# Optimization experiments

Hardware: AMD Instinct MI355X
Metric: run time of the kernel (lower is better)

Reference implementation:

```python
import jax, jax.numpy as jnp
import numpy as np

EPS = 1e-12  # matches torch F.normalize default eps (clamp_min)
B, C, N = 32, 512, 4096
K_CLUSTERS, G_CLUSTERS = 64, 8
T_CLUSTERS = K_CLUSTERS + G_CLUSTERS  # 72
H_ATTN = T_CLUSTERS // 4  # 18


def _l2norm(v, axis):
    return v / jnp.maximum(jnp.linalg.norm(v, axis=axis, keepdims=True), EPS)


def setup_inputs() -> dict:
    key = jax.random.key(0)
    ks = jax.random.split(key, 6)
    x = jax.random.normal(ks[0], (B, C, N), dtype=jnp.float32)
    centroids = jax.random.normal(ks[1], (T_CLUSTERS, C), dtype=jnp.float32) * 0.01
    # 1x1 Conv2d(C -> T) == dense [T, C] weight + bias
    conv_w = jax.random.normal(ks[2], (T_CLUSTERS, C), dtype=jnp.float32) / np.sqrt(C).astype(np.float32)
    conv_b = jnp.zeros((T_CLUSTERS,), dtype=jnp.float32)
    ghost_weights = jnp.ones((G_CLUSTERS,), dtype=jnp.float32) * 0.1
    w1 = jax.random.normal(ks[3], (H_ATTN, T_CLUSTERS), dtype=jnp.float32) / np.sqrt(T_CLUSTERS).astype(np.float32)
    b1 = jnp.zeros((H_ATTN,), dtype=jnp.float32)
    w2 = jax.random.normal(ks[4], (T_CLUSTERS, H_ATTN), dtype=jnp.float32) / np.sqrt(H_ATTN).astype(np.float32)
    b2 = jnp.zeros((T_CLUSTERS,), dtype=jnp.float32)
    return {"x": x, "centroids": centroids, "conv_w": conv_w, "conv_b": conv_b,
            "ghost_weights": ghost_weights, "w1": w1, "b1": b1, "w2": w2, "b2": b2}


def reference(x, centroids, conv_w, conv_b, ghost_weights, w1, b1, w2, b2):
    # x: [B, C, N] -> L2 normalize over channel dim
    xn = _l2norm(x, axis=1)
    # 1x1 conv -> soft assignment logits [B, T, N], softmax over clusters
    logits = jnp.einsum('kc,bcn->bkn', conv_w, xn) + conv_b[None, :, None]
    assign = jax.nn.softmax(logits, axis=1)
    # residual aggregation, algebraically fused:
    # vlad[b,k,c] = sum_n a[b,k,n]*x[b,c,n] - centroid[k,c]*sum_n a[b,k,n]
    agg = jnp.einsum('bkn,bcn->bkc', assign, xn)
    mass = assign.sum(axis=-1)  # [B, T]
    vlad = agg - centroids[None, :, :] * mass[:, :, None]
    # ghost cluster down-weighting
    gw = jax.nn.softmax(ghost_weights)
    vlad = vlad.at[:, K_CLUSTERS:, :].multiply(gw[None, :, None])
    # attention over clusters: mean over C -> MLP -> softmax over clusters
    scores = vlad.mean(axis=-1)  # [B, T]
    h = jax.nn.relu(scores @ w1.T + b1)
    attn = jax.nn.softmax(h @ w2.T + b2, axis=1)
    vlad = vlad * attn[:, :, None]
    # intra-cluster L2 norm, drop ghosts, flatten, global L2 norm
    vlad = _l2norm(vlad, axis=2)
    vlad = vlad[:, :K_CLUSTERS, :].reshape(vlad.shape[0], -1)
    return _l2norm(vlad, axis=1)
```

## Files before the change

### kernel.cpp

```cpp
#include <hip/hip_runtime.h>
#include <hip/hip_bf16.h>

#define B_ 32
#define C_ 512
#define N_ 4096
#define T_ 72
#define K_ 64
#define KP 80
#define EPSF 1e-12f

typedef unsigned short u16;
typedef unsigned int u32;
typedef __attribute__((ext_vector_type(8))) short bf16x8;
typedef __attribute__((ext_vector_type(4))) float f32x4;

__device__ __forceinline__ u16 f2bf(float v) {
    __hip_bfloat16 h = __float2bfloat16(v);
    return *reinterpret_cast<u16*>(&h);
}

__global__ __launch_bounds__(256) void k_prep(
    const float* __restrict__ conv_w, const float* __restrict__ conv_b,
    u16* __restrict__ Wp, float* __restrict__ bp)
{
    const int idx = blockIdx.x * 256 + threadIdx.x;
    if (idx < KP * C_) {
        const int k = idx >> 9, c = idx & (C_ - 1);
        Wp[idx] = f2bf(k < T_ ? conv_w[k * C_ + c] : 0.f);
    } else if (idx < KP * C_ + KP) {
        const int j = idx - KP * C_;
        bp[j] = (j < T_) ? conv_b[j] : -1e30f;
    }
}

#define ANW 256
__global__ __launch_bounds__(256, 2) void k_assign(
    const float* __restrict__ x, const u16* __restrict__ Wp,
    const float* __restrict__ bp, u16* __restrict__ assignp,
    float* __restrict__ mass)
{
    __shared__ u16   xs[ANW * 32];
    __shared__ float red[4][ANW];
    __shared__ float inv_sh[ANW];

    const int t = threadIdx.x;
    const int b = blockIdx.y;
    const int n0 = blockIdx.x * ANW;
    const int lane = t & 63, w = t >> 6;
    const int q = lane >> 4, nl = lane & 15;

    const float* xb = x + (size_t)b * C_ * N_ + n0 + 4 * lane;

    f32x4 acc[4][5];
    #pragma unroll
    for (int nt = 0; nt < 4; ++nt)
        #pragma unroll
        for (int mt = 0; mt < 5; ++mt) acc[nt][mt] = (f32x4)0.f;
    float ss[4] = {0.f, 0.f, 0.f, 0.f};

    float4 v[8];
    bf16x8 af[5];
    #pragma unroll
    for (int i = 0; i < 8; ++i)
        v[i] = *(const float4*)(xb + (size_t)(w * 8 + i) * N_);
    #pragma unroll
    for (int mt = 0; mt < 5; ++mt)
        af[mt] = *(const bf16x8*)(Wp + (size_t)(mt * 16 + nl) * C_ + q * 8);

#define VJ(i) (j == 0 ? v[i].x : j == 1 ? v[i].y : j == 2 ? v[i].z : v[i].w)

    #pragma unroll 1
    for (int ch = 0; ch < 16; ++ch) {
        #pragma unroll
        for (int j = 0; j < 4; ++j) {
            const float f0 = VJ(0), f1 = VJ(1), f2 = VJ(2), f3 = VJ(3);
            const float f4 = VJ(4), f5 = VJ(5), f6 = VJ(6), f7 = VJ(7);
            ss[j] = fmaf(f0, f0, ss[j]); ss[j] = fmaf(f1, f1, ss[j]);
            ss[j] = fmaf(f2, f2, ss[j]); ss[j] = fmaf(f3, f3, ss[j]);
            ss[j] = fmaf(f4, f4, ss[j]); ss[j] = fmaf(f5, f5, ss[j]);
            ss[j] = fmaf(f6, f6, ss[j]); ss[j] = fmaf(f7, f7, ss[j]);
            uint4 pk;
            pk.x = (u32)f2bf(f0) | ((u32)f2bf(f1) << 16);
            pk.y = (u32)f2bf(f2) | ((u32)f2bf(f3) << 16);
            pk.z = (u32)f2bf(f4) | ((u32)f2bf(f5) << 16);
            pk.w = (u32)f2bf(f6) | ((u32)f2bf(f7) << 16);
            const int n = 4 * lane + j;
            const int slot = (w + ((lane >> 1) & 3)) & 3;
            *(uint4*)&xs[n * 32 + slot * 8] = pk;
        }
        __syncthreads();
        if (ch < 15) {
            #pragma unroll
            for (int i = 0; i < 8; ++i)
                v[i] = *(const float4*)(xb + (size_t)((ch + 1) * 32 + w * 8 + i) * N_);
        }
        __builtin_amdgcn_sched_barrier(0);
        #pragma unroll
        for (int nt = 0; nt < 4; ++nt) {
            const int n = (4 * w + nt) * 16 + nl;
            const int slot = (q + ((n >> 3) & 3)) & 3;
            const bf16x8 bfr = *(const bf16x8*)&xs[n * 32 + slot * 8];
            #pragma unroll
            for (int mt = 0; mt < 5; ++mt)
                acc[nt][mt] = __builtin_amdgcn_mfma_f32_16x16x32_bf16(af[mt], bfr, acc[nt][mt], 0, 0, 0);
        }
        if (ch < 15) {
            #pragma unroll
            for (int mt = 0; mt < 5; ++mt)
                af[mt] = *(const bf16x8*)(Wp + (size_t)(mt * 16 + nl) * C_ + (ch + 1) * 32 + q * 8);
        }
        __syncthreads();
    }
#undef VJ

    *(float4*)&red[w][4 * lane] = make_float4(ss[0], ss[1], ss[2], ss[3]);
    __syncthreads();
    {
        const float s = red[0][t] + red[1][t] + red[2][t] + red[3][t];
        inv_sh[t] = 1.0f / fmaxf(sqrtf(s), EPSF);
    }
    __syncthreads();

    float bpv[5][4];
    #pragma unroll
    for (int mt = 0; mt < 5; ++mt)
        #pragma unroll
        for (int r = 0; r < 4; ++r) bpv[mt][r] = bp[mt * 16 + q * 4 + r];

    #pragma unroll
    for (int nt = 0; nt < 4; ++nt) {
        const int n_loc = (4 * w + nt) * 16 + nl;
        const float invn = inv_sh[n_loc];
        const int nglob = n0 + n_loc;

        float lg[5][4];
        #pragma unroll
        for (int mt = 0; mt < 5; ++mt)
            #pragma unroll
            for (int r = 0; r < 4; ++r)
                lg[mt][r] = acc[nt][mt][r] * invn + bpv[mt][r];

        float mx = -1e30f;
        #pragma unroll
        for (int mt = 0; mt < 5; ++mt)
            #pragma unroll
            for (int r = 0; r < 4; ++r) mx = fmaxf(mx, lg[mt][r]);
        mx = fmaxf(mx, __shfl_xor(mx, 16, 64));
        mx = fmaxf(mx, __shfl_xor(mx, 32, 64));

        float s = 0.f;
        #pragma unroll
        for (int mt = 0; mt < 5; ++mt)
            #pragma unroll
            for (int r = 0; r < 4; ++r) {
                lg[mt][r] = __expf(lg[mt][r] - mx);
                s += lg[mt][r];
            }
        s += __shfl_xor(s, 16, 64);
        s += __shfl_xor(s, 32, 64);
        const float rs = 1.0f / s;

        #pragma unroll
        for (int mt = 0; mt < 4; ++mt)
            #pragma unroll
            for (int r = 0; r < 4; ++r) {
                const float a = lg[mt][r] * rs;
                float msum = a;
                msum += __shfl_xor(msum, 1, 64);
                msum += __shfl_xor(msum, 2, 64);
                msum += __shfl_xor(msum, 4, 64);
                msum += __shfl_xor(msum, 8, 64);
                const int k = mt * 16 + q * 4 + r;
                if (nl == 0) atomicAdd(&mass[b * K_ + k], msum);
                assignp[((size_t)b * K_ + k) * N_ + nglob] = f2bf(a * invn);
            }
    }
}

#define AGW 1024
#define AGS 128
#define AGP 136
__global__ __launch_bounds__(256) void k_agg(
    const float* __restrict__ x, const u16* __restrict__ assignp,
    float* __restrict__ out)
{
    __shared__ u16 At[K_][AGP];
    __shared__ u16 Bt[K_][AGP];

    const int t = threadIdx.x, b = blockIdx.z;
    const int nc0 = blockIdx.y * AGW;
    const int c0 = blockIdx.x * 64;
    const int lane = t & 63, w = t >> 6;
    const int q = lane >> 4, nl = lane & 15;

    const int as = lane & 15, ar = lane >> 4;
    const int bs = lane & 31, br = lane >> 5;

    f32x4 acc[4];
    #pragma unroll
    for (int mt = 0; mt < 4; ++mt) acc[mt] = (f32x4)0.f;

    const u16*   ab = assignp + (size_t)b * K_ * N_;
    const float* xb = x + ((size_t)b * C_ + c0) * N_;

    uint4  ra[4];
    float4 rb[8];
    #pragma unroll
    for (int i = 0; i < 4; ++i)
        ra[i] = *(const uint4*)(ab + (size_t)(16 * w + 4 * i + ar) * N_ + nc0 + as * 8);
    #pragma unroll
    for (int i = 0; i < 8; ++i)
        rb[i] = *(const float4*)(xb + (size_t)(16 * w + 2 * i + br) * N_ + nc0 + bs * 4);

    #pragma unroll 1
    for (int ph = 0; ph < AGW / AGS; ++ph) {
        #pragma unroll
        for (int i = 0; i < 4; ++i)
            *(uint4*)&At[16 * w + 4 * i + ar][as * 8] = ra[i];
        #pragma unroll
        for (int i = 0; i < 8; ++i) {
            const float4 vv = rb[i];
            uint2 pk;
            pk.x = (u32)f2bf(vv.x) | ((u32)f2bf(vv.y) << 16);
            pk.y = (u32)f2bf(vv.z) | ((u32)f2bf(vv.w) << 16);
            *(uint2*)&Bt[16 * w + 2 * i + br][bs * 4] = pk;
        }
        __syncthreads();
        if (ph < AGW / AGS - 1) {
            const int n1 = nc0 + (ph + 1) * AGS;
            #pragma unroll
            for (int i = 0; i < 4; ++i)
                ra[i] = *(const uint4*)(ab + (size_t)(16 * w + 4 * i + ar) * N_ + n1 + as * 8);
            #pragma unroll
            for (int i = 0; i < 8; ++i)
                rb[i] = *(const float4*)(xb + (size_t)(16 * w + 2 * i + br) * N_ + n1 + bs * 4);
        }
        __builtin_amdgcn_sched_barrier(0);
        #pragma unroll
        for (int ks = 0; ks < 4; ++ks) {
            const bf16x8 bfr = *(const bf16x8*)&Bt[16 * w + nl][ks * 32 + q * 8];
            #pragma unroll
            for (int mt = 0; mt < 4; ++mt) {
                const bf16x8 afv = *(const bf16x8*)&At[mt * 16 + nl][ks * 32 + q * 8];
                acc[mt] = __builtin_amdgcn_mfma_f32_16x16x32_bf16(afv, bfr, acc[mt], 0, 0, 0);
            }
        }
        __syncthreads();
    }

    float* ob = out + (size_t)b * K_ * C_;
    const int c = c0 + 16 * w + nl;
    #pragma unroll
    for (int mt = 0; mt < 4; ++mt)
        #pragma unroll
        for (int r = 0; r < 4; ++r)
            atomicAdd(&ob[(size_t)(mt * 16 + q * 4 + r) * C_ + c], acc[mt][r]);
}

__device__ __forceinline__ float block_reduce_sum_256(float v) {
    #pragma unroll
    for (int o = 32; o > 0; o >>= 1) v += __shfl_down(v, o, 64);
    __shared__ float wsh[4];
    const int lane = threadIdx.x & 63, wid = threadIdx.x >> 6;
    if (lane == 0) wsh[wid] = v;
    __syncthreads();
    float r = 0.f;
    if (threadIdx.x == 0) r = wsh[0] + wsh[1] + wsh[2] + wsh[3];
    return r;
}

__global__ __launch_bounds__(256) void k_rnorm(
    const float* __restrict__ agg, const float* __restrict__ centroids,
    const float* __restrict__ mass, float* __restrict__ rnorm,
    float* __restrict__ gsum)
{
    const int k = blockIdx.x, b = blockIdx.y;
    const float mk = mass[b * K_ + k];
    const float* p  = agg + ((size_t)b * K_ + k) * C_;
    const float* cb = centroids + k * C_;
    float s = 0.f;
    #pragma unroll 2
    for (int i = threadIdx.x; i < C_; i += 256) {
        const float v = fmaf(-cb[i], mk, p[i]);
        s = fmaf(v, v, s);
    }
    const float ss = block_reduce_sum_256(s);
    if (threadIdx.x == 0) {
        const float rn = fmaxf(sqrtf(ss), EPSF);
        rnorm[b * K_ + k] = rn;
        atomicAdd(gsum + b, ss / (rn * rn));
    }
}

__global__ __launch_bounds__(256) void k_final(
    float* __restrict__ out, const float* __restrict__ centroids,
    const float* __restrict__ mass, const float* __restrict__ rnorm,
    const float* __restrict__ gsum)
{
    const size_t i4 = ((size_t)blockIdx.x * 256 + threadIdx.x) * 4;
    const int b = (int)(i4 >> 15);
    const int k = (int)((i4 >> 9) & 63);
    const int c = (int)(i4 & 511);
    const float gn = fmaxf(sqrtf(gsum[b]), EPSF);
    const float sc = 1.0f / (rnorm[b * K_ + k] * gn);
    const float mk = mass[b * K_ + k];
    float4 v  = *(const float4*)(out + i4);
    const float4 cv = *(const float4*)(centroids + k * C_ + c);
    v.x = fmaf(-cv.x, mk, v.x) * sc;
    v.y = fmaf(-cv.y, mk, v.y) * sc;
    v.z = fmaf(-cv.z, mk, v.z) * sc;
    v.w = fmaf(-cv.w, mk, v.w) * sc;
    *(float4*)(out + i4) = v;
}

extern "C" void kernel_launch(void* const* d_in, const int* in_sizes, int n_in,
                              void* d_out, int out_size, void* d_ws, size_t ws_size,
                              hipStream_t stream) {
    const float* x         = (const float*)d_in[0];
    const float* centroids = (const float*)d_in[1];
    const float* conv_w    = (const float*)d_in[2];
    const float* conv_b    = (const float*)d_in[3];

    float* out = (float*)d_out;
    char*  ws  = (char*)d_ws;

    u16*   assignp = (u16*)ws;
    u16*   Wp      = (u16*)(ws + 16777216);
    float* bpad    = (float*)(ws + 16777216 + 81920);
    float* mass    = (float*)(ws + 16777216 + 81920 + 320);
    float* rnorm   = mass + B_ * K_;
    float* gsum    = rnorm + B_ * K_;

    hipMemsetAsync(mass, 0, B_ * K_ * sizeof(float), stream);
    hipMemsetAsync(gsum, 0, B_ * sizeof(float), stream);
    hipMemsetAsync(out, 0, (size_t)out_size * sizeof(float), stream);

    k_prep<<<dim3((KP * C_ + KP + 255) / 256), 256, 0, stream>>>(conv_w, conv_b, Wp, bpad);
    k_assign<<<dim3(N_ / ANW, B_), 256, 0, stream>>>(x, Wp, bpad, assignp, mass);
    k_agg<<<dim3(C_ / 64, N_ / AGW, B_), 256, 0, stream>>>(x, assignp, out);
    k_rnorm<<<dim3(K_, B_), 256, 0, stream>>>(out, centroids, mass, rnorm, gsum);
    k_final<<<(out_size / 4 + 255) / 256, 256, 0, stream>>>(out, centroids, mass, rnorm, gsum);
}
```

Before: 517.0 us.

## Write bf16 copy of x in assign pass, fuse memsets and norm kernels

The assignment kernel now also writes a bf16 copy of x to workspace, so the aggregation kernel reads half the bytes and skips its fp32-to-bf16 conversion. The three memsets are folded into the prep kernel, and the rnorm and final kernels are merged into one per-batch kernel that keeps per-cluster norms in registers. This removes launches and global atomics, but adds a 128MB bf16 write. The merged norm kernel runs only 32 blocks, which limits its parallelism.

```diff
diff --git a/kernel.cpp b/kernel.cpp
--- a/kernel.cpp
+++ b/kernel.cpp
@@ -21,9 +21,15 @@
 
 __global__ __launch_bounds__(256) void k_prep(
     const float* __restrict__ conv_w, const float* __restrict__ conv_b,
-    u16* __restrict__ Wp, float* __restrict__ bp)
+    u16* __restrict__ Wp, float* __restrict__ bp,
+    float* __restrict__ out, float* __restrict__ mass)
 {
     const int idx = blockIdx.x * 256 + threadIdx.x;
+    if (idx < (B_ * K_ * C_) / 4)
+        ((float4*)out)[idx] = make_float4(0.f, 0.f, 0.f, 0.f);
+    else if (idx < (B_ * K_ * C_) / 4 + B_ * K_)
+        mass[idx - (B_ * K_ * C_) / 4] = 0.f;
+
     if (idx < KP * C_) {
         const int k = idx >> 9, c = idx & (C_ - 1);
         Wp[idx] = f2bf(k < T_ ? conv_w[k * C_ + c] : 0.f);
@@ -37,7 +43,7 @@
 __global__ __launch_bounds__(256, 2) void k_assign(
     const float* __restrict__ x, const u16* __restrict__ Wp,
     const float* __restrict__ bp, u16* __restrict__ assignp,
-    float* __restrict__ mass)
+    u16* __restrict__ xbf, float* __restrict__ mass)
 {
     __shared__ u16   xs[ANW * 32];
     __shared__ float red[4][ANW];
@@ -71,6 +77,13 @@
 
     #pragma unroll 1
     for (int ch = 0; ch < 16; ++ch) {
+        #pragma unroll
+        for (int i = 0; i < 8; ++i) {
+            uint2 px;
+            px.x = (u32)f2bf(v[i].x) | ((u32)f2bf(v[i].y) << 16);
+            px.y = (u32)f2bf(v[i].z) | ((u32)f2bf(v[i].w) << 16);
+            *(uint2*)(xbf + ((size_t)b * C_ + ch * 32 + w * 8 + i) * N_ + n0 + 4 * lane) = px;
+        }
         #pragma unroll
         for (int j = 0; j < 4; ++j) {
             const float f0 = VJ(0), f1 = VJ(1), f2 = VJ(2), f3 = VJ(3);
@@ -181,7 +194,7 @@
 #define AGS 128
 #define AGP 136
 __global__ __launch_bounds__(256) void k_agg(
-    const float* __restrict__ x, const u16* __restrict__ assignp,
+    const u16* __restrict__ xbf, const u16* __restrict__ assignp,
     float* __restrict__ out)
 {
     __shared__ u16 At[K_][AGP];
@@ -194,46 +207,36 @@
     const int q = lane >> 4, nl = lane & 15;
 
     const int as = lane & 15, ar = lane >> 4;
-    const int bs = lane & 31, br = lane >> 5;
 
     f32x4 acc[4];
     #pragma unroll
     for (int mt = 0; mt < 4; ++mt) acc[mt] = (f32x4)0.f;
 
-    const u16*   ab = assignp + (size_t)b * K_ * N_;
-    const float* xb = x + ((size_t)b * C_ + c0) * N_;
-
-    uint4  ra[4];
-    float4 rb[8];
-    #pragma unroll
-    for (int i = 0; i < 4; ++i)
-        ra[i] = *(const uint4*)(ab + (size_t)(16 * w + 4 * i + ar) * N_ + nc0 + as * 8);
-    #pragma unroll
-    for (int i = 0; i < 8; ++i)
-        rb[i] = *(const float4*)(xb + (size_t)(16 * w + 2 * i + br) * N_ + nc0 + bs * 4);
+    const u16* ab  = assignp + (size_t)b * K_ * N_;
+    const u16* xbb = xbf + ((size_t)b * C_ + c0) * N_;
+
+    uint4 ra[4], rb[4];
+    #pragma unroll
+    for (int i = 0; i < 4; ++i) {
+        ra[i] = *(const uint4*)(ab  + (size_t)(16 * w + 4 * i + ar) * N_ + nc0 + as * 8);
+        rb[i] = *(const uint4*)(xbb + (size_t)(16 * w + 4 * i + ar) * N_ + nc0 + as * 8);
+    }
 
     #pragma unroll 1
     for (int ph = 0; ph < AGW / AGS; ++ph) {
         #pragma unroll
-        for (int i = 0; i < 4; ++i)
+        for (int i = 0; i < 4; ++i) {
             *(uint4*)&At[16 * w + 4 * i + ar][as * 8] = ra[i];
-        #pragma unroll
-        for (int i = 0; i < 8; ++i) {
-            const float4 vv = rb[i];
-            uint2 pk;
-            pk.x = (u32)f2bf(vv.x) | ((u32)f2bf(vv.y) << 16);
-            pk.y = (u32)f2bf(vv.z) | ((u32)f2bf(vv.w) << 16);
-            *(uint2*)&Bt[16 * w + 2 * i + br][bs * 4] = pk;
+            *(uint4*)&Bt[16 * w + 4 * i + ar][as * 8] = rb[i];
         }
         __syncthreads();
         if (ph < AGW / AGS - 1) {
             const int n1 = nc0 + (ph + 1) * AGS;
             #pragma unroll
-            for (int i = 0; i < 4; ++i)
-                ra[i] = *(const uint4*)(ab + (size_t)(16 * w + 4 * i + ar) * N_ + n1 + as * 8);
-            #pragma unroll
-            for (int i = 0; i < 8; ++i)
-                rb[i] = *(const float4*)(xb + (size_t)(16 * w + 2 * i + br) * N_ + n1 + bs * 4);
+            for (int i = 0; i < 4; ++i) {
+                ra[i] = *(const uint4*)(ab  + (size_t)(16 * w + 4 * i + ar) * N_ + n1 + as * 8);
+                rb[i] = *(const uint4*)(xbb + (size_t)(16 * w + 4 * i + ar) * N_ + n1 + as * 8);
+            }
         }
         __builtin_amdgcn_sched_barrier(0);
         #pragma unroll
@@ -257,60 +260,66 @@
             atomicAdd(&ob[(size_t)(mt * 16 + q * 4 + r) * C_ + c], acc[mt][r]);
 }
 
-__device__ __forceinline__ float block_reduce_sum_256(float v) {
-    #pragma unroll
-    for (int o = 32; o > 0; o >>= 1) v += __shfl_down(v, o, 64);
-    __shared__ float wsh[4];
-    const int lane = threadIdx.x & 63, wid = threadIdx.x >> 6;
-    if (lane == 0) wsh[wid] = v;
+__global__ __launch_bounds__(256) void k_norm(
+    float* __restrict__ out, const float* __restrict__ centroids,
+    const float* __restrict__ mass)
+{
+    const int b = blockIdx.x;
+    const int t = threadIdx.x, lane = t & 63, w = t >> 6;
+    __shared__ float gw[4];
+
+    float* ob = out + (size_t)b * K_ * C_;
+    float rn_r[16];
+    float gacc = 0.f;
+
+    #pragma unroll
+    for (int i = 0; i < 16; ++i) {
+        const int k = w + 4 * i;
+        const float mk = mass[b * K_ + k];
+        const float4 c0 = *(const float4*)(centroids + k * C_ + lane * 8);
+        const float4 c1 = *(const float4*)(centroids + k * C_ + lane * 8 + 4);
+        const float4 p0 = *(const float4*)(ob + k * C_ + lane * 8);
+        const float4 p1 = *(const float4*)(ob + k * C_ + lane * 8 + 4);
+        float vv, s;
+        vv = fmaf(-c0.x, mk, p0.x); s  = vv * vv;
+        vv = fmaf(-c0.y, mk, p0.y); s += vv * vv;
+        vv = fmaf(-c0.z, mk, p0.z); s += vv * vv;
+        vv = fmaf(-c0.w, mk, p0.w); s += vv * vv;
+        vv = fmaf(-c1.x, mk, p1.x); s += vv * vv;
+        vv = fmaf(-c1.y, mk, p1.y); s += vv * vv;
+        vv = fmaf(-c1.z, mk, p1.z); s += vv * vv;
+        vv = fmaf(-c1.w, mk, p1.w); s += vv * vv;
+        #pragma unroll
+        for (int o = 32; o > 0; o >>= 1) s += __shfl_down(s, o, 64);
+        s = __shfl(s, 0, 64);
+        const float rn = fmaxf(sqrtf(s), EPSF);
+        rn_r[i] = rn;
+        gacc += s / (rn * rn);
+    }
+    if (lane == 0) gw[w] = gacc;
     __syncthreads();
-    float r = 0.f;
-    if (threadIdx.x == 0) r = wsh[0] + wsh[1] + wsh[2] + wsh[3];
-    return r;
-}
-
-__global__ __launch_bounds__(256) void k_rnorm(
-    const float* __restrict__ agg, const float* __restrict__ centroids,
-    const float* __restrict__ mass, float* __restrict__ rnorm,
-    float* __restrict__ gsum)
-{
-    const int k = blockIdx.x, b = blockIdx.y;
-    const float mk = mass[b * K_ + k];
-    const float* p  = agg + ((size_t)b * K_ + k) * C_;
-    const float* cb = centroids + k * C_;
-    float s = 0.f;
-    #pragma unroll 2
-    for (int i = threadIdx.x; i < C_; i += 256) {
-        const float v = fmaf(-cb[i], mk, p[i]);
-        s = fmaf(v, v, s);
-    }
-    const float ss = block_reduce_sum_256(s);
-    if (threadIdx.x == 0) {
-        const float rn = fmaxf(sqrtf(ss), EPSF);
-        rnorm[b * K_ + k] = rn;
-        atomicAdd(gsum + b, ss / (rn * rn));
-    }
-}
-
-__global__ __launch_bounds__(256) void k_final(
-    float* __restrict__ out, const float* __restrict__ centroids,
-    const float* __restrict__ mass, const float* __restrict__ rnorm,
-    const float* __restrict__ gsum)
-{
-    const size_t i4 = ((size_t)blockIdx.x * 256 + threadIdx.x) * 4;
-    const int b = (int)(i4 >> 15);
-    const int k = (int)((i4 >> 9) & 63);
-    const int c = (int)(i4 & 511);
-    const float gn = fmaxf(sqrtf(gsum[b]), EPSF);
-    const float sc = 1.0f / (rnorm[b * K_ + k] * gn);
-    const float mk = mass[b * K_ + k];
-    float4 v  = *(const float4*)(out + i4);
-    const float4 cv = *(const float4*)(centroids + k * C_ + c);
-    v.x = fmaf(-cv.x, mk, v.x) * sc;
-    v.y = fmaf(-cv.y, mk, v.y) * sc;
-    v.z = fmaf(-cv.z, mk, v.z) * sc;
-    v.w = fmaf(-cv.w, mk, v.w) * sc;
-    *(float4*)(out + i4) = v;
+    const float gn = fmaxf(sqrtf(gw[0] + gw[1] + gw[2] + gw[3]), EPSF);
+
+    #pragma unroll
+    for (int i = 0; i < 16; ++i) {
+        const int k = w + 4 * i;
+        const float mk = mass[b * K_ + k];
+        const float sc = 1.0f / (rn_r[i] * gn);
+        const float4 c0 = *(const float4*)(centroids + k * C_ + lane * 8);
+        const float4 c1 = *(const float4*)(centroids + k * C_ + lane * 8 + 4);
+        float4 p0 = *(const float4*)(ob + k * C_ + lane * 8);
+        float4 p1 = *(const float4*)(ob + k * C_ + lane * 8 + 4);
+        p0.x = fmaf(-c0.x, mk, p0.x) * sc;
+        p0.y = fmaf(-c0.y, mk, p0.y) * sc;
+        p0.z = fmaf(-c0.z, mk, p0.z) * sc;
+        p0.w = fmaf(-c0.w, mk, p0.w) * sc;
+        p1.x = fmaf(-c1.x, mk, p1.x) * sc;
+        p1.y = fmaf(-c1.y, mk, p1.y) * sc;
+        p1.z = fmaf(-c1.z, mk, p1.z) * sc;
+        p1.w = fmaf(-c1.w, mk, p1.w) * sc;
+        *(float4*)(ob + k * C_ + lane * 8)     = p0;
+        *(float4*)(ob + k * C_ + lane * 8 + 4) = p1;
+    }
 }
 
 extern "C" void kernel_launch(void* const* d_in, const int* in_sizes, int n_in,
@@ -328,16 +337,11 @@
     u16*   Wp      = (u16*)(ws + 16777216);
     float* bpad    = (float*)(ws + 16777216 + 81920);
     float* mass    = (float*)(ws + 16777216 + 81920 + 320);
-    float* rnorm   = mass + B_ * K_;
-    float* gsum    = rnorm + B_ * K_;
-
-    hipMemsetAsync(mass, 0, B_ * K_ * sizeof(float), stream);
-    hipMemsetAsync(gsum, 0, B_ * sizeof(float), stream);
-    hipMemsetAsync(out, 0, (size_t)out_size * sizeof(float), stream);
-
-    k_prep<<<dim3((KP * C_ + KP + 255) / 256), 256, 0, stream>>>(conv_w, conv_b, Wp, bpad);
-    k_assign<<<dim3(N_ / ANW, B_), 256, 0, stream>>>(x, Wp, bpad, assignp, mass);
-    k_agg<<<dim3(C_ / 64, N_ / AGW, B_), 256, 0, stream>>>(x, assignp, out);
-    k_rnorm<<<dim3(K_, B_), 256, 0, stream>>>(out, centroids, mass, rnorm, gsum);
-    k_final<<<(out_size / 4 + 255) / 256, 256, 0, stream>>>(out, centroids, mass, rnorm, gsum);
-}
+    u16*   xbf     = (u16*)(ws + 33554432);
+
+    k_prep<<<dim3(((B_ * K_ * C_) / 4 + B_ * K_ + 255) / 256), 256, 0, stream>>>(
+        conv_w, conv_b, Wp, bpad, out, mass);
+    k_assign<<<dim3(N_ / ANW, B_), 256, 0, stream>>>(x, Wp, bpad, assignp, xbf, mass);
+    k_agg<<<dim3(C_ / 64, N_ / AGW, B_), 256, 0, stream>>>(xbf, assignp, out);
+    k_norm<<<dim3(B_), 256, 0, stream>>>(out, centroids, mass);
+}
```

Result: slower. 560.5 us (+8.4%).
